# Kernel optimization log

Measured on AMD Instinct MI355X. Metric: run time of the kernel, lower is better.

## Reference

```python
import jax, jax.numpy as jnp
import numpy as np

B, N, F_IN, F_OUT, H = 8, 1024, 256, 256, 4
HD = F_OUT // H  # head_dim = 64
NEG_SLOPE = 0.2


def setup_inputs() -> dict:
    key = jax.random.key(0)
    k1, k2, k3 = jax.random.split(key, 3)
    x = jax.random.normal(k1, (B, N, F_IN), dtype=jnp.float32)
    adj = jnp.ones((B, N, N), dtype=jnp.int32)
    # Linear weight, stored as [in, out] so h = x @ W
    W = jax.random.normal(k2, (F_IN, F_OUT), dtype=jnp.float32) / np.sqrt(F_IN)
    # attention vector a: [H, 2*head_dim], xavier-ish init
    a = jax.random.normal(k3, (H, 2 * HD), dtype=jnp.float32) * np.sqrt(2.0 / (H + 2 * HD))
    return {"x": x, "adj": adj, "W": W, "a": a}


def reference(x, adj, W, a):
    Bq, Nq, _ = x.shape
    h = (x @ W).reshape(Bq, Nq, H, HD).transpose(0, 2, 1, 3)  # [B,H,N,HD]
    a1, a2 = a[:, :HD], a[:, HD:]  # decompose concat: e_nm = h_n.a1 + h_m.a2
    s1 = jnp.einsum('bhnd,hd->bhn', h, a1)
    s2 = jnp.einsum('bhmd,hd->bhm', h, a2)
    e = jax.nn.leaky_relu(s1[:, :, :, None] + s2[:, :, None, :], NEG_SLOPE)  # [B,H,N,N]
    e = jnp.where(adj[:, None, :, :] == 0, -jnp.inf, e)
    attention = jax.nn.softmax(e, axis=-1)
    out = jnp.einsum('bhnm,bhmd->bhnd', attention, h)
    return out.transpose(0, 2, 1, 3).reshape(Bq, Nq, H * HD)
```

## Files before the change

### kernel.cpp

```cpp
#include <hip/hip_runtime.h>
#include <math.h>

#define H 4
#define HD 64
#define NN 1024
#define BB 8
#define FIN 256
#define FOUT 256

typedef _Float16 f16x8 __attribute__((ext_vector_type(8)));
typedef _Float16 f16x4 __attribute__((ext_vector_type(4)));
typedef _Float16 f16x2 __attribute__((ext_vector_type(2)));
typedef float f32x4 __attribute__((ext_vector_type(4)));

__global__ __launch_bounds__(256) void prep(const int* __restrict__ adj,
                                            unsigned* __restrict__ adjP,
                                            const float* __restrict__ W,
                                            _Float16* __restrict__ WT) {
  __shared__ float tile[64][68];
  const int tid = threadIdx.x;
  if (blockIdx.x < 1024) {
    size_t widx = (size_t)blockIdx.x * 256 + tid;
    const int4* p = (const int4*)adj + widx * 8;
    int4 v[8];
#pragma unroll
    for (int i = 0; i < 8; ++i) v[i] = p[i];
    unsigned bits = 0;
#pragma unroll
    for (int i = 0; i < 8; ++i) {
      bits |= (v[i].x != 0 ? 1u : 0u) << (4 * i);
      bits |= (v[i].y != 0 ? 2u : 0u) << (4 * i);
      bits |= (v[i].z != 0 ? 4u : 0u) << (4 * i);
      bits |= (v[i].w != 0 ? 8u : 0u) << (4 * i);
    }
    adjP[widx] = bits;
  } else {
    const int bx = blockIdx.x - 1024;
    const int k0 = (bx & 3) * 64, f0 = (bx >> 2) * 64;
    const int r = tid >> 4, c4 = (tid & 15) * 4;
#pragma unroll
    for (int p = 0; p < 4; ++p) {
      float4 v = *(const float4*)&W[(size_t)(k0 + p * 16 + r) * FOUT + f0 + c4];
      *(float4*)&tile[p * 16 + r][c4] = v;
    }
    __syncthreads();
    const int f = tid >> 2, kg = (tid & 3) * 16;
#pragma unroll
    for (int i = 0; i < 4; ++i) {
      f16x4 o;
#pragma unroll
      for (int j = 0; j < 4; ++j) o[j] = (_Float16)tile[kg + i * 4 + j][f];
      *(f16x4*)&WT[(size_t)(f0 + f) * FIN + k0 + kg + i * 4] = o;
    }
  }
}

__global__ __launch_bounds__(256) void gemm_xw(const float* __restrict__ x,
                                               const _Float16* __restrict__ WT,
                                               const float* __restrict__ a,
                                               _Float16* __restrict__ hT,
                                               float* __restrict__ s1_ws,
                                               float* __restrict__ s2_ws,
                                               float* __restrict__ u_ws,
                                               float* __restrict__ v_ws) {
  __shared__ _Float16 xs[64][264];
  const int tid = threadIdx.x;
  const int lane = tid & 63, w = tid >> 6;
  const int c = lane & 15, q = lane >> 4;
  const int bn0 = blockIdx.x * 64;
  const int head = blockIdx.y;
  const int b = bn0 >> 10, nb = bn0 & 1023;
  const int bh = b * H + head;

  float4 v[16];
#pragma unroll
  for (int p = 0; p < 16; ++p) {
    int f = p * 256 + tid;
    int row = f >> 6, col = (f & 63) * 4;
    v[p] = *(const float4*)&x[(size_t)(bn0 + row) * FIN + col];
  }
#pragma unroll
  for (int p = 0; p < 16; ++p) {
    int f = p * 256 + tid;
    int row = f >> 6, col = (f & 63) * 4;
    f16x4 h4;
    h4[0] = (_Float16)v[p].x; h4[1] = (_Float16)v[p].y;
    h4[2] = (_Float16)v[p].z; h4[3] = (_Float16)v[p].w;
    *(f16x4*)&xs[row][col] = h4;
  }
  __syncthreads();

  f32x4 acc[4];
#pragma unroll
  for (int t = 0; t < 4; ++t) acc[t] = (f32x4){0.f, 0.f, 0.f, 0.f};
  const _Float16* wbase = WT + (size_t)head * 64 * FIN;
#pragma unroll
  for (int ks = 0; ks < 8; ++ks) {
    f16x8 af = *(const f16x8*)&xs[w * 16 + c][ks * 32 + q * 8];
#pragma unroll
    for (int t = 0; t < 4; ++t) {
      f16x8 bf = *(const f16x8*)&wbase[(size_t)(t * 16 + c) * FIN + ks * 32 + q * 8];
      acc[t] = __builtin_amdgcn_mfma_f32_16x16x32_f16(af, bf, acc[t], 0, 0, 0);
    }
  }

  float a1v[4], a2v[4];
#pragma unroll
  for (int t = 0; t < 4; ++t) {
    a1v[t] = a[head * 2 * HD + t * 16 + c];
    a2v[t] = a[head * 2 * HD + HD + t * 16 + c];
  }
  float s1p[4] = {0.f, 0.f, 0.f, 0.f};
  float s2p[4] = {0.f, 0.f, 0.f, 0.f};
#pragma unroll
  for (int t = 0; t < 4; ++t) {
    f16x4 hv;
#pragma unroll
    for (int rr = 0; rr < 4; ++rr) {
      hv[rr] = (_Float16)acc[t][rr];
      s1p[rr] += acc[t][rr] * a1v[t];
      s2p[rr] += acc[t][rr] * a2v[t];
    }
    *(f16x4*)&hT[((size_t)(bh * 64 + t * 16 + c)) * NN + nb + w * 16 + q * 4] = hv;
  }
#pragma unroll
  for (int rr = 0; rr < 4; ++rr) {
    float s1 = s1p[rr], s2 = s2p[rr];
#pragma unroll
    for (int off = 8; off; off >>= 1) {
      s1 += __shfl_xor(s1, off);
      s2 += __shfl_xor(s2, off);
    }
    if (c == 0) {
      int n = nb + w * 16 + q * 4 + rr;
      size_t idx = (size_t)bh * NN + n;
      s1_ws[idx] = s1;
      s2_ws[idx] = s2;
      u_ws[idx] = __expf(s2);
      v_ws[idx] = __expf(0.2f * s2);
    }
  }
}

__global__ __launch_bounds__(256) void attn(const _Float16* __restrict__ hT,
                                            const float* __restrict__ s1_ws,
                                            const float* __restrict__ s2_ws,
                                            const float* __restrict__ u_ws,
                                            const float* __restrict__ v_ws,
                                            const unsigned* __restrict__ adjP,
                                            float* __restrict__ out) {
  __shared__ float s2r[NN], uu[NN], vv[NN];
  __shared__ _Float16 pt[2][32][136];
  __shared__ unsigned adjW[32][32];
  __shared__ float invL[32];
  const int tid = threadIdx.x, lane = tid & 63, w = tid >> 6;
  const int c = lane & 15, q = lane >> 4;
  const int ntile = blockIdx.x, bh = blockIdx.y;
  const int b = bh >> 2, head = bh & 3;
  const int n0 = ntile * 32;

  {
    size_t base = (size_t)bh * NN + tid * 4;
    *(float4*)&s2r[tid * 4] = *(const float4*)&s2_ws[base];
    *(float4*)&uu[tid * 4] = *(const float4*)&u_ws[base];
    *(float4*)&vv[tid * 4] = *(const float4*)&v_ws[base];
    uint4 aw = *(const uint4*)&adjP[((size_t)(b * NN + n0)) * 32 + tid * 4];
    *(uint4*)&adjW[tid >> 3][(tid * 4) & 31] = aw;
  }
  __syncthreads();

  float s1v[8];
#pragma unroll
  for (int r = 0; r < 8; ++r) s1v[r] = s1_ws[(size_t)bh * NN + n0 + w * 8 + r];

  const int wc = lane >> 4;
  const int shft = (2 * lane) & 31;

  float mx[8];
#pragma unroll
  for (int r = 0; r < 8; ++r) mx[r] = -INFINITY;
#pragma unroll
  for (int ch = 0; ch < 8; ++ch) {
    float2 s2p = *(const float2*)&s2r[ch * 128 + 2 * lane];
#pragma unroll
    for (int r = 0; r < 8; ++r) {
      unsigned bits = adjW[w * 8 + r][ch * 4 + wc] >> shft;
      mx[r] = fmaxf(mx[r], (bits & 1u) ? s2p.x : -INFINITY);
      mx[r] = fmaxf(mx[r], (bits & 2u) ? s2p.y : -INFINITY);
    }
  }
  float Arow[8], Brow[8], ns1[8];
#pragma unroll
  for (int r = 0; r < 8; ++r) {
    float m = mx[r];
#pragma unroll
    for (int off = 32; off; off >>= 1) m = fmaxf(m, __shfl_xor(m, off));
    float t0 = s1v[r] + m;
    float M = fmaxf(t0, 0.2f * t0);
    Arow[r] = __expf(s1v[r] - M);
    Brow[r] = __expf(0.2f * s1v[r] - M);
    ns1[r] = -s1v[r];
  }

  float Lp[8];
#pragma unroll
  for (int r = 0; r < 8; ++r) Lp[r] = 0.f;
  f32x4 acc[2];
  acc[0] = (f32x4){0.f, 0.f, 0.f, 0.f};
  acc[1] = (f32x4){0.f, 0.f, 0.f, 0.f};
  const _Float16* bptr = hT + ((size_t)bh * 64 + w * 16 + c) * NN + q * 8;

  f16x8 nbf0 = *(const f16x8*)(bptr);
  f16x8 nbf1 = *(const f16x8*)(bptr + 32);
  f16x8 nbf2 = *(const f16x8*)(bptr + 64);
  f16x8 nbf3 = *(const f16x8*)(bptr + 96);

  for (int ch = 0; ch < 8; ++ch) {
    const int buf = ch & 1;
    f16x8 bf0 = nbf0, bf1 = nbf1, bf2 = nbf2, bf3 = nbf3;
    float2 s2p = *(const float2*)&s2r[ch * 128 + 2 * lane];
    float2 up = *(const float2*)&uu[ch * 128 + 2 * lane];
    float2 vp = *(const float2*)&vv[ch * 128 + 2 * lane];
#pragma unroll
    for (int r = 0; r < 8; ++r) {
      unsigned bits = adjW[w * 8 + r][ch * 4 + wc] >> shft;
      float p0 = (s2p.x >= ns1[r]) ? Arow[r] * up.x : Brow[r] * vp.x;
      float p1 = (s2p.y >= ns1[r]) ? Arow[r] * up.y : Brow[r] * vp.y;
      p0 = (bits & 1u) ? p0 : 0.f;
      p1 = (bits & 2u) ? p1 : 0.f;
      Lp[r] += p0 + p1;
      f16x2 pk = __builtin_bit_cast(f16x2, __builtin_amdgcn_cvt_pkrtz(p0, p1));
      *(f16x2*)&pt[buf][w * 8 + r][2 * lane] = pk;
    }
    if (ch < 7) {
      nbf0 = *(const f16x8*)(bptr + (ch + 1) * 128);
      nbf1 = *(const f16x8*)(bptr + (ch + 1) * 128 + 32);
      nbf2 = *(const f16x8*)(bptr + (ch + 1) * 128 + 64);
      nbf3 = *(const f16x8*)(bptr + (ch + 1) * 128 + 96);
    }
    __syncthreads();
#pragma unroll
    for (int t = 0; t < 2; ++t) {
      f16x8 a0 = *(const f16x8*)&pt[buf][t * 16 + c][q * 8];
      f16x8 a1 = *(const f16x8*)&pt[buf][t * 16 + c][32 + q * 8];
      f16x8 a2 = *(const f16x8*)&pt[buf][t * 16 + c][64 + q * 8];
      f16x8 a3 = *(const f16x8*)&pt[buf][t * 16 + c][96 + q * 8];
      acc[t] = __builtin_amdgcn_mfma_f32_16x16x32_f16(a0, bf0, acc[t], 0, 0, 0);
      acc[t] = __builtin_amdgcn_mfma_f32_16x16x32_f16(a1, bf1, acc[t], 0, 0, 0);
      acc[t] = __builtin_amdgcn_mfma_f32_16x16x32_f16(a2, bf2, acc[t], 0, 0, 0);
      acc[t] = __builtin_amdgcn_mfma_f32_16x16x32_f16(a3, bf3, acc[t], 0, 0, 0);
    }
  }

  float myL = 0.f;
#pragma unroll
  for (int r = 0; r < 8; ++r) {
    float s = Lp[r];
#pragma unroll
    for (int off = 32; off; off >>= 1) s += __shfl_xor(s, off);
    if (lane == r) myL = s;
  }
  if (lane < 8) invL[w * 8 + lane] = 1.0f / myL;
  __syncthreads();
#pragma unroll
  for (int t = 0; t < 2; ++t) {
#pragma unroll
    for (int rr = 0; rr < 4; ++rr) {
      int nloc = t * 16 + q * 4 + rr;
      out[((size_t)(b * NN + n0 + nloc)) * FOUT + head * 64 + w * 16 + c] =
          acc[t][rr] * invL[nloc];
    }
  }
}

extern "C" void kernel_launch(void* const* d_in, const int* in_sizes, int n_in,
                              void* d_out, int out_size, void* d_ws, size_t ws_size,
                              hipStream_t stream) {
  const float* x = (const float*)d_in[0];
  const int* adj = (const int*)d_in[1];
  const float* W = (const float*)d_in[2];
  const float* a = (const float*)d_in[3];
  float* out = (float*)d_out;

  char* ws = (char*)d_ws;
  _Float16* hT = (_Float16*)ws;
  _Float16* WT = (_Float16*)(ws + (size_t)4 * 1024 * 1024);
  float* s1_ws = (float*)(ws + (size_t)4 * 1024 * 1024 + 128 * 1024);
  float* s2_ws = s1_ws + (size_t)BB * H * NN;
  float* u_ws = s2_ws + (size_t)BB * H * NN;
  float* v_ws = u_ws + (size_t)BB * H * NN;
  unsigned* adjP = (unsigned*)(v_ws + (size_t)BB * H * NN);

  prep<<<1040, 256, 0, stream>>>(adj, adjP, W, WT);
  gemm_xw<<<dim3(128, 4), 256, 0, stream>>>(x, WT, a, hT, s1_ws, s2_ws, u_ws, v_ws);
  attn<<<dim3(32, 32), 256, 0, stream>>>(hT, s1_ws, s2_ws, u_ws, v_ws, adjP, out);
}
```

Baseline: 118.8 us.

## Fuse adjacency bit-packing into attention kernel and load x directly into registers

```diff
diff --git a/kernel.cpp b/kernel.cpp
--- a/kernel.cpp
+++ b/kernel.cpp
@@ -13,45 +13,26 @@
 typedef _Float16 f16x2 __attribute__((ext_vector_type(2)));
 typedef float f32x4 __attribute__((ext_vector_type(4)));
 
-__global__ __launch_bounds__(256) void prep(const int* __restrict__ adj,
-                                            unsigned* __restrict__ adjP,
-                                            const float* __restrict__ W,
-                                            _Float16* __restrict__ WT) {
+__global__ __launch_bounds__(256) void prep_w(const float* __restrict__ W,
+                                              _Float16* __restrict__ WT) {
   __shared__ float tile[64][68];
   const int tid = threadIdx.x;
-  if (blockIdx.x < 1024) {
-    size_t widx = (size_t)blockIdx.x * 256 + tid;
-    const int4* p = (const int4*)adj + widx * 8;
-    int4 v[8];
-#pragma unroll
-    for (int i = 0; i < 8; ++i) v[i] = p[i];
-    unsigned bits = 0;
-#pragma unroll
-    for (int i = 0; i < 8; ++i) {
-      bits |= (v[i].x != 0 ? 1u : 0u) << (4 * i);
-      bits |= (v[i].y != 0 ? 2u : 0u) << (4 * i);
-      bits |= (v[i].z != 0 ? 4u : 0u) << (4 * i);
-      bits |= (v[i].w != 0 ? 8u : 0u) << (4 * i);
-    }
-    adjP[widx] = bits;
-  } else {
-    const int bx = blockIdx.x - 1024;
-    const int k0 = (bx & 3) * 64, f0 = (bx >> 2) * 64;
-    const int r = tid >> 4, c4 = (tid & 15) * 4;
-#pragma unroll
-    for (int p = 0; p < 4; ++p) {
-      float4 v = *(const float4*)&W[(size_t)(k0 + p * 16 + r) * FOUT + f0 + c4];
-      *(float4*)&tile[p * 16 + r][c4] = v;
-    }
-    __syncthreads();
-    const int f = tid >> 2, kg = (tid & 3) * 16;
-#pragma unroll
-    for (int i = 0; i < 4; ++i) {
-      f16x4 o;
-#pragma unroll
-      for (int j = 0; j < 4; ++j) o[j] = (_Float16)tile[kg + i * 4 + j][f];
-      *(f16x4*)&WT[(size_t)(f0 + f) * FIN + k0 + kg + i * 4] = o;
-    }
+  const int bx = blockIdx.x;
+  const int k0 = (bx & 3) * 64, f0 = (bx >> 2) * 64;
+  const int r = tid >> 4, c4 = (tid & 15) * 4;
+#pragma unroll
+  for (int p = 0; p < 4; ++p) {
+    float4 v = *(const float4*)&W[(size_t)(k0 + p * 16 + r) * FOUT + f0 + c4];
+    *(float4*)&tile[p * 16 + r][c4] = v;
+  }
+  __syncthreads();
+  const int f = tid >> 2, kg = (tid & 3) * 16;
+#pragma unroll
+  for (int i = 0; i < 4; ++i) {
+    f16x4 o;
+#pragma unroll
+    for (int j = 0; j < 4; ++j) o[j] = (_Float16)tile[kg + i * 4 + j][f];
+    *(f16x4*)&WT[(size_t)(f0 + f) * FIN + k0 + kg + i * 4] = o;
   }
 }
 
@@ -63,7 +44,6 @@
                                                float* __restrict__ s2_ws,
                                                float* __restrict__ u_ws,
                                                float* __restrict__ v_ws) {
-  __shared__ _Float16 xs[64][264];
   const int tid = threadIdx.x;
   const int lane = tid & 63, w = tid >> 6;
   const int c = lane & 15, q = lane >> 4;
@@ -72,31 +52,28 @@
   const int b = bn0 >> 10, nb = bn0 & 1023;
   const int bh = b * H + head;
 
-  float4 v[16];
-#pragma unroll
-  for (int p = 0; p < 16; ++p) {
-    int f = p * 256 + tid;
-    int row = f >> 6, col = (f & 63) * 4;
-    v[p] = *(const float4*)&x[(size_t)(bn0 + row) * FIN + col];
-  }
-#pragma unroll
-  for (int p = 0; p < 16; ++p) {
-    int f = p * 256 + tid;
-    int row = f >> 6, col = (f & 63) * 4;
-    f16x4 h4;
-    h4[0] = (_Float16)v[p].x; h4[1] = (_Float16)v[p].y;
-    h4[2] = (_Float16)v[p].z; h4[3] = (_Float16)v[p].w;
-    *(f16x4*)&xs[row][col] = h4;
-  }
-  __syncthreads();
+  const _Float16* wbase = WT + (size_t)head * 64 * FIN;
+  const float* xrow = x + (size_t)(bn0 + w * 16 + c) * FIN;
+
+  float4 xa[16];
+#pragma unroll
+  for (int ks = 0; ks < 8; ++ks) {
+    xa[2 * ks] = *(const float4*)&xrow[ks * 32 + q * 8];
+    xa[2 * ks + 1] = *(const float4*)&xrow[ks * 32 + q * 8 + 4];
+  }
 
   f32x4 acc[4];
 #pragma unroll
   for (int t = 0; t < 4; ++t) acc[t] = (f32x4){0.f, 0.f, 0.f, 0.f};
-  const _Float16* wbase = WT + (size_t)head * 64 * FIN;
+
 #pragma unroll
   for (int ks = 0; ks < 8; ++ks) {
-    f16x8 af = *(const f16x8*)&xs[w * 16 + c][ks * 32 + q * 8];
+    float4 u0 = xa[2 * ks], u1 = xa[2 * ks + 1];
+    f16x8 af;
+    af[0] = (_Float16)u0.x; af[1] = (_Float16)u0.y;
+    af[2] = (_Float16)u0.z; af[3] = (_Float16)u0.w;
+    af[4] = (_Float16)u1.x; af[5] = (_Float16)u1.y;
+    af[6] = (_Float16)u1.z; af[7] = (_Float16)u1.w;
 #pragma unroll
     for (int t = 0; t < 4; ++t) {
       f16x8 bf = *(const f16x8*)&wbase[(size_t)(t * 16 + c) * FIN + ks * 32 + q * 8];
@@ -147,7 +124,7 @@
                                             const float* __restrict__ s2_ws,
                                             const float* __restrict__ u_ws,
                                             const float* __restrict__ v_ws,
-                                            const unsigned* __restrict__ adjP,
+                                            const int* __restrict__ adj,
                                             float* __restrict__ out) {
   __shared__ float s2r[NN], uu[NN], vv[NN];
   __shared__ _Float16 pt[2][32][136];
@@ -164,8 +141,27 @@
     *(float4*)&s2r[tid * 4] = *(const float4*)&s2_ws[base];
     *(float4*)&uu[tid * 4] = *(const float4*)&u_ws[base];
     *(float4*)&vv[tid * 4] = *(const float4*)&v_ws[base];
-    uint4 aw = *(const uint4*)&adjP[((size_t)(b * NN + n0)) * 32 + tid * 4];
-    *(uint4*)&adjW[tid >> 3][(tid * 4) & 31] = aw;
+  }
+  {
+    const int row = tid >> 3, seg = tid & 7;
+    const int4* ap = (const int4*)&adj[((size_t)(b * NN + n0 + row)) * NN + seg * 128];
+    unsigned wds[4];
+#pragma unroll
+    for (int wi = 0; wi < 4; ++wi) {
+      int4 vb[8];
+#pragma unroll
+      for (int i = 0; i < 8; ++i) vb[i] = ap[wi * 8 + i];
+      unsigned bits = 0;
+#pragma unroll
+      for (int i = 0; i < 8; ++i) {
+        bits |= (vb[i].x != 0 ? 1u : 0u) << (4 * i);
+        bits |= (vb[i].y != 0 ? 2u : 0u) << (4 * i);
+        bits |= (vb[i].z != 0 ? 4u : 0u) << (4 * i);
+        bits |= (vb[i].w != 0 ? 8u : 0u) << (4 * i);
+      }
+      wds[wi] = bits;
+    }
+    *(uint4*)&adjW[row][seg * 4] = make_uint4(wds[0], wds[1], wds[2], wds[3]);
   }
   __syncthreads();
 
@@ -289,9 +285,8 @@
   float* s2_ws = s1_ws + (size_t)BB * H * NN;
   float* u_ws = s2_ws + (size_t)BB * H * NN;
   float* v_ws = u_ws + (size_t)BB * H * NN;
-  unsigned* adjP = (unsigned*)(v_ws + (size_t)BB * H * NN);
-
-  prep<<<1040, 256, 0, stream>>>(adj, adjP, W, WT);
+
+  prep_w<<<16, 256, 0, stream>>>(W, WT);
   gemm_xw<<<dim3(128, 4), 256, 0, stream>>>(x, WT, a, hT, s1_ws, s2_ws, u_ws, v_ws);
-  attn<<<dim3(32, 32), 256, 0, stream>>>(hT, s1_ws, s2_ws, u_ws, v_ws, adjP, out);
-}
+  attn<<<dim3(32, 32), 256, 0, stream>>>(hT, s1_ws, s2_ws, u_ws, v_ws, adj, out);
+}
```

New measurement: 129.1 us. +8.6%, slower.

## Halve attention row tile to 16 and recompute exp(s2) in-kernel

Applied to the files above, without the earlier changes.

```diff
diff --git a/kernel.cpp b/kernel.cpp
--- a/kernel.cpp
+++ b/kernel.cpp
@@ -60,9 +60,7 @@
                                                const float* __restrict__ a,
                                                _Float16* __restrict__ hT,
                                                float* __restrict__ s1_ws,
-                                               float* __restrict__ s2_ws,
-                                               float* __restrict__ u_ws,
-                                               float* __restrict__ v_ws) {
+                                               float* __restrict__ s2_ws) {
   __shared__ _Float16 xs[64][264];
   const int tid = threadIdx.x;
   const int lane = tid & 63, w = tid >> 6;
@@ -136,8 +134,6 @@
       size_t idx = (size_t)bh * NN + n;
       s1_ws[idx] = s1;
       s2_ws[idx] = s2;
-      u_ws[idx] = __expf(s2);
-      v_ws[idx] = __expf(0.2f * s2);
     }
   }
 }
@@ -145,53 +141,48 @@
 __global__ __launch_bounds__(256) void attn(const _Float16* __restrict__ hT,
                                             const float* __restrict__ s1_ws,
                                             const float* __restrict__ s2_ws,
-                                            const float* __restrict__ u_ws,
-                                            const float* __restrict__ v_ws,
                                             const unsigned* __restrict__ adjP,
                                             float* __restrict__ out) {
-  __shared__ float s2r[NN], uu[NN], vv[NN];
-  __shared__ _Float16 pt[2][32][136];
-  __shared__ unsigned adjW[32][32];
-  __shared__ float invL[32];
+  __shared__ float s2r[NN];
+  __shared__ _Float16 pt[2][16][136];
+  __shared__ unsigned adjW[16][32];
+  __shared__ float invL[16];
   const int tid = threadIdx.x, lane = tid & 63, w = tid >> 6;
   const int c = lane & 15, q = lane >> 4;
   const int ntile = blockIdx.x, bh = blockIdx.y;
   const int b = bh >> 2, head = bh & 3;
-  const int n0 = ntile * 32;
-
-  {
-    size_t base = (size_t)bh * NN + tid * 4;
-    *(float4*)&s2r[tid * 4] = *(const float4*)&s2_ws[base];
-    *(float4*)&uu[tid * 4] = *(const float4*)&u_ws[base];
-    *(float4*)&vv[tid * 4] = *(const float4*)&v_ws[base];
+  const int n0 = ntile * 16;
+
+  *(float4*)&s2r[tid * 4] = *(const float4*)&s2_ws[(size_t)bh * NN + tid * 4];
+  if (tid < 128) {
     uint4 aw = *(const uint4*)&adjP[((size_t)(b * NN + n0)) * 32 + tid * 4];
     *(uint4*)&adjW[tid >> 3][(tid * 4) & 31] = aw;
   }
   __syncthreads();
 
-  float s1v[8];
-#pragma unroll
-  for (int r = 0; r < 8; ++r) s1v[r] = s1_ws[(size_t)bh * NN + n0 + w * 8 + r];
+  float s1v[4];
+#pragma unroll
+  for (int r = 0; r < 4; ++r) s1v[r] = s1_ws[(size_t)bh * NN + n0 + w * 4 + r];
 
   const int wc = lane >> 4;
   const int shft = (2 * lane) & 31;
 
-  float mx[8];
-#pragma unroll
-  for (int r = 0; r < 8; ++r) mx[r] = -INFINITY;
+  float mx[4];
+#pragma unroll
+  for (int r = 0; r < 4; ++r) mx[r] = -INFINITY;
 #pragma unroll
   for (int ch = 0; ch < 8; ++ch) {
     float2 s2p = *(const float2*)&s2r[ch * 128 + 2 * lane];
 #pragma unroll
-    for (int r = 0; r < 8; ++r) {
-      unsigned bits = adjW[w * 8 + r][ch * 4 + wc] >> shft;
+    for (int r = 0; r < 4; ++r) {
+      unsigned bits = adjW[w * 4 + r][ch * 4 + wc] >> shft;
       mx[r] = fmaxf(mx[r], (bits & 1u) ? s2p.x : -INFINITY);
       mx[r] = fmaxf(mx[r], (bits & 2u) ? s2p.y : -INFINITY);
     }
   }
-  float Arow[8], Brow[8], ns1[8];
-#pragma unroll
-  for (int r = 0; r < 8; ++r) {
+  float Arow[4], Brow[4], ns1[4];
+#pragma unroll
+  for (int r = 0; r < 4; ++r) {
     float m = mx[r];
 #pragma unroll
     for (int off = 32; off; off >>= 1) m = fmaxf(m, __shfl_xor(m, off));
@@ -202,12 +193,8 @@
     ns1[r] = -s1v[r];
   }
 
-  float Lp[8];
-#pragma unroll
-  for (int r = 0; r < 8; ++r) Lp[r] = 0.f;
-  f32x4 acc[2];
-  acc[0] = (f32x4){0.f, 0.f, 0.f, 0.f};
-  acc[1] = (f32x4){0.f, 0.f, 0.f, 0.f};
+  float Lp[4] = {0.f, 0.f, 0.f, 0.f};
+  f32x4 acc = (f32x4){0.f, 0.f, 0.f, 0.f};
   const _Float16* bptr = hT + ((size_t)bh * 64 + w * 16 + c) * NN + q * 8;
 
   f16x8 nbf0 = *(const f16x8*)(bptr);
@@ -219,18 +206,18 @@
     const int buf = ch & 1;
     f16x8 bf0 = nbf0, bf1 = nbf1, bf2 = nbf2, bf3 = nbf3;
     float2 s2p = *(const float2*)&s2r[ch * 128 + 2 * lane];
-    float2 up = *(const float2*)&uu[ch * 128 + 2 * lane];
-    float2 vp = *(const float2*)&vv[ch * 128 + 2 * lane];
-#pragma unroll
-    for (int r = 0; r < 8; ++r) {
-      unsigned bits = adjW[w * 8 + r][ch * 4 + wc] >> shft;
-      float p0 = (s2p.x >= ns1[r]) ? Arow[r] * up.x : Brow[r] * vp.x;
-      float p1 = (s2p.y >= ns1[r]) ? Arow[r] * up.y : Brow[r] * vp.y;
+    float ux = __expf(s2p.x), uy = __expf(s2p.y);
+    float vx = __expf(0.2f * s2p.x), vy = __expf(0.2f * s2p.y);
+#pragma unroll
+    for (int r = 0; r < 4; ++r) {
+      unsigned bits = adjW[w * 4 + r][ch * 4 + wc] >> shft;
+      float p0 = (s2p.x >= ns1[r]) ? Arow[r] * ux : Brow[r] * vx;
+      float p1 = (s2p.y >= ns1[r]) ? Arow[r] * uy : Brow[r] * vy;
       p0 = (bits & 1u) ? p0 : 0.f;
       p1 = (bits & 2u) ? p1 : 0.f;
       Lp[r] += p0 + p1;
       f16x2 pk = __builtin_bit_cast(f16x2, __builtin_amdgcn_cvt_pkrtz(p0, p1));
-      *(f16x2*)&pt[buf][w * 8 + r][2 * lane] = pk;
+      *(f16x2*)&pt[buf][w * 4 + r][2 * lane] = pk;
     }
     if (ch < 7) {
       nbf0 = *(const f16x8*)(bptr + (ch + 1) * 128);
@@ -239,37 +226,31 @@
       nbf3 = *(const f16x8*)(bptr + (ch + 1) * 128 + 96);
     }
     __syncthreads();
-#pragma unroll
-    for (int t = 0; t < 2; ++t) {
-      f16x8 a0 = *(const f16x8*)&pt[buf][t * 16 + c][q * 8];
-      f16x8 a1 = *(const f16x8*)&pt[buf][t * 16 + c][32 + q * 8];
-      f16x8 a2 = *(const f16x8*)&pt[buf][t * 16 + c][64 + q * 8];
-      f16x8 a3 = *(const f16x8*)&pt[buf][t * 16 + c][96 + q * 8];
-      acc[t] = __builtin_amdgcn_mfma_f32_16x16x32_f16(a0, bf0, acc[t], 0, 0, 0);
-      acc[t] = __builtin_amdgcn_mfma_f32_16x16x32_f16(a1, bf1, acc[t], 0, 0, 0);
-      acc[t] = __builtin_amdgcn_mfma_f32_16x16x32_f16(a2, bf2, acc[t], 0, 0, 0);
-      acc[t] = __builtin_amdgcn_mfma_f32_16x16x32_f16(a3, bf3, acc[t], 0, 0, 0);
-    }
+    f16x8 a0 = *(const f16x8*)&pt[buf][c][q * 8];
+    f16x8 a1 = *(const f16x8*)&pt[buf][c][32 + q * 8];
+    f16x8 a2 = *(const f16x8*)&pt[buf][c][64 + q * 8];
+    f16x8 a3 = *(const f16x8*)&pt[buf][c][96 + q * 8];
+    acc = __builtin_amdgcn_mfma_f32_16x16x32_f16(a0, bf0, acc, 0, 0, 0);
+    acc = __builtin_amdgcn_mfma_f32_16x16x32_f16(a1, bf1, acc, 0, 0, 0);
+    acc = __builtin_amdgcn_mfma_f32_16x16x32_f16(a2, bf2, acc, 0, 0, 0);
+    acc = __builtin_amdgcn_mfma_f32_16x16x32_f16(a3, bf3, acc, 0, 0, 0);
   }
 
   float myL = 0.f;
 #pragma unroll
-  for (int r = 0; r < 8; ++r) {
+  for (int r = 0; r < 4; ++r) {
     float s = Lp[r];
 #pragma unroll
     for (int off = 32; off; off >>= 1) s += __shfl_xor(s, off);
     if (lane == r) myL = s;
   }
-  if (lane < 8) invL[w * 8 + lane] = 1.0f / myL;
+  if (lane < 4) invL[w * 4 + lane] = 1.0f / myL;
   __syncthreads();
 #pragma unroll
-  for (int t = 0; t < 2; ++t) {
-#pragma unroll
-    for (int rr = 0; rr < 4; ++rr) {
-      int nloc = t * 16 + q * 4 + rr;
-      out[((size_t)(b * NN + n0 + nloc)) * FOUT + head * 64 + w * 16 + c] =
-          acc[t][rr] * invL[nloc];
-    }
+  for (int rr = 0; rr < 4; ++rr) {
+    int nloc = q * 4 + rr;
+    out[((size_t)(b * NN + n0 + nloc)) * FOUT + head * 64 + w * 16 + c] =
+        acc[rr] * invL[nloc];
   }
 }
 
@@ -287,11 +268,9 @@
   _Float16* WT = (_Float16*)(ws + (size_t)4 * 1024 * 1024);
   float* s1_ws = (float*)(ws + (size_t)4 * 1024 * 1024 + 128 * 1024);
   float* s2_ws = s1_ws + (size_t)BB * H * NN;
-  float* u_ws = s2_ws + (size_t)BB * H * NN;
-  float* v_ws = u_ws + (size_t)BB * H * NN;
-  unsigned* adjP = (unsigned*)(v_ws + (size_t)BB * H * NN);
+  unsigned* adjP = (unsigned*)(s2_ws + (size_t)BB * H * NN);
 
   prep<<<1040, 256, 0, stream>>>(adj, adjP, W, WT);
-  gemm_xw<<<dim3(128, 4), 256, 0, stream>>>(x, WT, a, hT, s1_ws, s2_ws, u_ws, v_ws);
-  attn<<<dim3(32, 32), 256, 0, stream>>>(hT, s1_ws, s2_ws, u_ws, v_ws, adjP, out);
-}
+  gemm_xw<<<dim3(128, 4), 256, 0, stream>>>(x, WT, a, hT, s1_ws, s2_ws);
+  attn<<<dim3(64, 32), 256, 0, stream>>>(hT, s1_ws, s2_ws, adjP, out);
+}
```

Result: slower. 129.2 us (+8.7%).

## Split attention over key dimension across waves with register-resident P operands

Applied to the files above, without the earlier changes.

```diff
diff --git a/kernel.cpp b/kernel.cpp
--- a/kernel.cpp
+++ b/kernel.cpp
@@ -150,125 +150,175 @@
                                             const unsigned* __restrict__ adjP,
                                             float* __restrict__ out) {
   __shared__ float s2r[NN], uu[NN], vv[NN];
-  __shared__ _Float16 pt[2][32][136];
-  __shared__ unsigned adjW[32][32];
-  __shared__ float invL[32];
+  __shared__ unsigned adjT[32][32];
+  __shared__ float accbuf[2][2][4][64][4];
+  __shared__ float Mbuf[4][32];
+  __shared__ float Lbuf[4][32];
+  __shared__ float invLb[32];
   const int tid = threadIdx.x, lane = tid & 63, w = tid >> 6;
   const int c = lane & 15, q = lane >> 4;
   const int ntile = blockIdx.x, bh = blockIdx.y;
   const int b = bh >> 2, head = bh & 3;
   const int n0 = ntile * 32;
+  const int K0 = w * 256, W0 = w * 8;
 
   {
     size_t base = (size_t)bh * NN + tid * 4;
     *(float4*)&s2r[tid * 4] = *(const float4*)&s2_ws[base];
     *(float4*)&uu[tid * 4] = *(const float4*)&u_ws[base];
     *(float4*)&vv[tid * 4] = *(const float4*)&v_ws[base];
-    uint4 aw = *(const uint4*)&adjP[((size_t)(b * NN + n0)) * 32 + tid * 4];
-    *(uint4*)&adjW[tid >> 3][(tid * 4) & 31] = aw;
-  }
-  __syncthreads();
-
-  float s1v[8];
-#pragma unroll
-  for (int r = 0; r < 8; ++r) s1v[r] = s1_ws[(size_t)bh * NN + n0 + w * 8 + r];
-
-  const int wc = lane >> 4;
-  const int shft = (2 * lane) & 31;
-
-  float mx[8];
-#pragma unroll
-  for (int r = 0; r < 8; ++r) mx[r] = -INFINITY;
-#pragma unroll
-  for (int ch = 0; ch < 8; ++ch) {
-    float2 s2p = *(const float2*)&s2r[ch * 128 + 2 * lane];
-#pragma unroll
-    for (int r = 0; r < 8; ++r) {
-      unsigned bits = adjW[w * 8 + r][ch * 4 + wc] >> shft;
-      mx[r] = fmaxf(mx[r], (bits & 1u) ? s2p.x : -INFINITY);
-      mx[r] = fmaxf(mx[r], (bits & 2u) ? s2p.y : -INFINITY);
-    }
-  }
-  float Arow[8], Brow[8], ns1[8];
-#pragma unroll
-  for (int r = 0; r < 8; ++r) {
-    float m = mx[r];
-#pragma unroll
-    for (int off = 32; off; off >>= 1) m = fmaxf(m, __shfl_xor(m, off));
-    float t0 = s1v[r] + m;
-    float M = fmaxf(t0, 0.2f * t0);
-    Arow[r] = __expf(s1v[r] - M);
-    Brow[r] = __expf(0.2f * s1v[r] - M);
-    ns1[r] = -s1v[r];
-  }
-
-  float Lp[8];
-#pragma unroll
-  for (int r = 0; r < 8; ++r) Lp[r] = 0.f;
-  f32x4 acc[2];
-  acc[0] = (f32x4){0.f, 0.f, 0.f, 0.f};
-  acc[1] = (f32x4){0.f, 0.f, 0.f, 0.f};
-  const _Float16* bptr = hT + ((size_t)bh * 64 + w * 16 + c) * NN + q * 8;
-
-  f16x8 nbf0 = *(const f16x8*)(bptr);
-  f16x8 nbf1 = *(const f16x8*)(bptr + 32);
-  f16x8 nbf2 = *(const f16x8*)(bptr + 64);
-  f16x8 nbf3 = *(const f16x8*)(bptr + 96);
-
-  for (int ch = 0; ch < 8; ++ch) {
-    const int buf = ch & 1;
-    f16x8 bf0 = nbf0, bf1 = nbf1, bf2 = nbf2, bf3 = nbf3;
-    float2 s2p = *(const float2*)&s2r[ch * 128 + 2 * lane];
-    float2 up = *(const float2*)&uu[ch * 128 + 2 * lane];
-    float2 vp = *(const float2*)&vv[ch * 128 + 2 * lane];
-#pragma unroll
-    for (int r = 0; r < 8; ++r) {
-      unsigned bits = adjW[w * 8 + r][ch * 4 + wc] >> shft;
-      float p0 = (s2p.x >= ns1[r]) ? Arow[r] * up.x : Brow[r] * vp.x;
-      float p1 = (s2p.y >= ns1[r]) ? Arow[r] * up.y : Brow[r] * vp.y;
-      p0 = (bits & 1u) ? p0 : 0.f;
-      p1 = (bits & 2u) ? p1 : 0.f;
-      Lp[r] += p0 + p1;
-      f16x2 pk = __builtin_bit_cast(f16x2, __builtin_amdgcn_cvt_pkrtz(p0, p1));
-      *(f16x2*)&pt[buf][w * 8 + r][2 * lane] = pk;
-    }
-    if (ch < 7) {
-      nbf0 = *(const f16x8*)(bptr + (ch + 1) * 128);
-      nbf1 = *(const f16x8*)(bptr + (ch + 1) * 128 + 32);
-      nbf2 = *(const f16x8*)(bptr + (ch + 1) * 128 + 64);
-      nbf3 = *(const f16x8*)(bptr + (ch + 1) * 128 + 96);
-    }
-    __syncthreads();
+    const int row = tid >> 3, wd0 = (tid & 7) * 4;
+    uint4 aw = *(const uint4*)&adjP[((size_t)(b * NN + n0 + row)) * 32 + wd0];
+    adjT[wd0 + 0][row] = aw.x;
+    adjT[wd0 + 1][row] = aw.y;
+    adjT[wd0 + 2][row] = aw.z;
+    adjT[wd0 + 3][row] = aw.w;
+  }
+  float s1A = s1_ws[(size_t)bh * NN + n0 + c];
+  float s1B = s1_ws[(size_t)bh * NN + n0 + 16 + c];
+  __syncthreads();
+
+  float mxA = -INFINITY, mxB = -INFINITY;
+#pragma unroll
+  for (int ks = 0; ks < 8; ++ks) {
+    int m0 = K0 + ks * 32 + q * 8;
+    f32x4 sa = *(const f32x4*)&s2r[m0];
+    f32x4 sb = *(const f32x4*)&s2r[m0 + 4];
+    unsigned wdA = adjT[W0 + ks][c] >> (q * 8);
+    unsigned wdB = adjT[W0 + ks][c + 16] >> (q * 8);
+#pragma unroll
+    for (int j = 0; j < 4; ++j) {
+      mxA = fmaxf(mxA, ((wdA >> j) & 1u) ? sa[j] : -INFINITY);
+      mxA = fmaxf(mxA, ((wdA >> (j + 4)) & 1u) ? sb[j] : -INFINITY);
+      mxB = fmaxf(mxB, ((wdB >> j) & 1u) ? sa[j] : -INFINITY);
+      mxB = fmaxf(mxB, ((wdB >> (j + 4)) & 1u) ? sb[j] : -INFINITY);
+    }
+  }
+  mxA = fmaxf(mxA, __shfl_xor(mxA, 16));
+  mxA = fmaxf(mxA, __shfl_xor(mxA, 32));
+  mxB = fmaxf(mxB, __shfl_xor(mxB, 16));
+  mxB = fmaxf(mxB, __shfl_xor(mxB, 32));
+  if (lane < 16) {
+    Mbuf[w][c] = mxA;
+    Mbuf[w][16 + c] = mxB;
+  }
+  __syncthreads();
+  float mrowA = fmaxf(fmaxf(Mbuf[0][c], Mbuf[1][c]), fmaxf(Mbuf[2][c], Mbuf[3][c]));
+  float mrowB = fmaxf(fmaxf(Mbuf[0][16 + c], Mbuf[1][16 + c]),
+                      fmaxf(Mbuf[2][16 + c], Mbuf[3][16 + c]));
+  float tA = s1A + mrowA, tB = s1B + mrowB;
+  float MA = fmaxf(tA, 0.2f * tA);
+  float MB = fmaxf(tB, 0.2f * tB);
+  float ArowA = __expf(s1A - MA), BrowA = __expf(0.2f * s1A - MA), ns1A = -s1A;
+  float ArowB = __expf(s1B - MB), BrowB = __expf(0.2f * s1B - MB), ns1B = -s1B;
+
+  float LpA = 0.f, LpB = 0.f;
+  f32x4 acc[2][4];
+#pragma unroll
+  for (int t = 0; t < 2; ++t)
+#pragma unroll
+    for (int d = 0; d < 4; ++d) acc[t][d] = (f32x4){0.f, 0.f, 0.f, 0.f};
+  const _Float16* hbase = hT + (size_t)bh * 64 * NN + (size_t)c * NN + K0 + q * 8;
+
+#pragma unroll 2
+  for (int ks = 0; ks < 8; ++ks) {
+    f16x8 bf0 = *(const f16x8*)(hbase + (size_t)0 * 16 * NN + ks * 32);
+    f16x8 bf1 = *(const f16x8*)(hbase + (size_t)1 * 16 * NN + ks * 32);
+    f16x8 bf2 = *(const f16x8*)(hbase + (size_t)2 * 16 * NN + ks * 32);
+    f16x8 bf3 = *(const f16x8*)(hbase + (size_t)3 * 16 * NN + ks * 32);
+
+    int m0 = K0 + ks * 32 + q * 8;
+    f32x4 sa = *(const f32x4*)&s2r[m0];
+    f32x4 sb = *(const f32x4*)&s2r[m0 + 4];
+    f32x4 ua = *(const f32x4*)&uu[m0];
+    f32x4 ub = *(const f32x4*)&uu[m0 + 4];
+    f32x4 va = *(const f32x4*)&vv[m0];
+    f32x4 vb = *(const f32x4*)&vv[m0 + 4];
+    unsigned wdA = adjT[W0 + ks][c] >> (q * 8);
+    unsigned wdB = adjT[W0 + ks][c + 16] >> (q * 8);
+
+    float pA[8], pB[8];
+#pragma unroll
+    for (int j = 0; j < 4; ++j) {
+      float a0 = (sa[j] >= ns1A) ? ArowA * ua[j] : BrowA * va[j];
+      float a1 = (sb[j] >= ns1A) ? ArowA * ub[j] : BrowA * vb[j];
+      pA[j] = ((wdA >> j) & 1u) ? a0 : 0.f;
+      pA[j + 4] = ((wdA >> (j + 4)) & 1u) ? a1 : 0.f;
+      float b0 = (sa[j] >= ns1B) ? ArowB * ua[j] : BrowB * va[j];
+      float b1 = (sb[j] >= ns1B) ? ArowB * ub[j] : BrowB * vb[j];
+      pB[j] = ((wdB >> j) & 1u) ? b0 : 0.f;
+      pB[j + 4] = ((wdB >> (j + 4)) & 1u) ? b1 : 0.f;
+    }
+    LpA += ((pA[0] + pA[1]) + (pA[2] + pA[3])) + ((pA[4] + pA[5]) + (pA[6] + pA[7]));
+    LpB += ((pB[0] + pB[1]) + (pB[2] + pB[3])) + ((pB[4] + pB[5]) + (pB[6] + pB[7]));
+
+    union { f16x8 v8; f16x2 h2[4]; } PA, PB;
+#pragma unroll
+    for (int j = 0; j < 4; ++j) {
+      PA.h2[j] = __builtin_bit_cast(f16x2, __builtin_amdgcn_cvt_pkrtz(pA[2 * j], pA[2 * j + 1]));
+      PB.h2[j] = __builtin_bit_cast(f16x2, __builtin_amdgcn_cvt_pkrtz(pB[2 * j], pB[2 * j + 1]));
+    }
+
+    acc[0][0] = __builtin_amdgcn_mfma_f32_16x16x32_f16(PA.v8, bf0, acc[0][0], 0, 0, 0);
+    acc[0][1] = __builtin_amdgcn_mfma_f32_16x16x32_f16(PA.v8, bf1, acc[0][1], 0, 0, 0);
+    acc[0][2] = __builtin_amdgcn_mfma_f32_16x16x32_f16(PA.v8, bf2, acc[0][2], 0, 0, 0);
+    acc[0][3] = __builtin_amdgcn_mfma_f32_16x16x32_f16(PA.v8, bf3, acc[0][3], 0, 0, 0);
+    acc[1][0] = __builtin_amdgcn_mfma_f32_16x16x32_f16(PB.v8, bf0, acc[1][0], 0, 0, 0);
+    acc[1][1] = __builtin_amdgcn_mfma_f32_16x16x32_f16(PB.v8, bf1, acc[1][1], 0, 0, 0);
+    acc[1][2] = __builtin_amdgcn_mfma_f32_16x16x32_f16(PB.v8, bf2, acc[1][2], 0, 0, 0);
+    acc[1][3] = __builtin_amdgcn_mfma_f32_16x16x32_f16(PB.v8, bf3, acc[1][3], 0, 0, 0);
+  }
+
+  LpA += __shfl_xor(LpA, 16);
+  LpA += __shfl_xor(LpA, 32);
+  LpB += __shfl_xor(LpB, 16);
+  LpB += __shfl_xor(LpB, 32);
+  if (lane < 16) {
+    Lbuf[w][c] = LpA;
+    Lbuf[w][16 + c] = LpB;
+  }
+  if (w >= 2) {
+#pragma unroll
+    for (int t = 0; t < 2; ++t)
+#pragma unroll
+      for (int d = 0; d < 4; ++d)
+        *(f32x4*)&accbuf[w - 2][t][d][lane][0] = acc[t][d];
+  }
+  __syncthreads();
+  if (w < 2) {
+#pragma unroll
+    for (int t = 0; t < 2; ++t)
+#pragma unroll
+      for (int d = 0; d < 4; ++d)
+        acc[t][d] += *(const f32x4*)&accbuf[w][t][d][lane][0];
+  }
+  if (tid < 32) {
+    float Ls = Lbuf[0][tid] + Lbuf[1][tid] + Lbuf[2][tid] + Lbuf[3][tid];
+    invLb[tid] = 1.0f / Ls;
+  }
+  __syncthreads();
+  if (w == 1) {
+#pragma unroll
+    for (int t = 0; t < 2; ++t)
+#pragma unroll
+      for (int d = 0; d < 4; ++d)
+        *(f32x4*)&accbuf[0][t][d][lane][0] = acc[t][d];
+  }
+  __syncthreads();
+  if (w == 0) {
 #pragma unroll
     for (int t = 0; t < 2; ++t) {
-      f16x8 a0 = *(const f16x8*)&pt[buf][t * 16 + c][q * 8];
-      f16x8 a1 = *(const f16x8*)&pt[buf][t * 16 + c][32 + q * 8];
-      f16x8 a2 = *(const f16x8*)&pt[buf][t * 16 + c][64 + q * 8];
-      f16x8 a3 = *(const f16x8*)&pt[buf][t * 16 + c][96 + q * 8];
-      acc[t] = __builtin_amdgcn_mfma_f32_16x16x32_f16(a0, bf0, acc[t], 0, 0, 0);
-      acc[t] = __builtin_amdgcn_mfma_f32_16x16x32_f16(a1, bf1, acc[t], 0, 0, 0);
-      acc[t] = __builtin_amdgcn_mfma_f32_16x16x32_f16(a2, bf2, acc[t], 0, 0, 0);
-      acc[t] = __builtin_amdgcn_mfma_f32_16x16x32_f16(a3, bf3, acc[t], 0, 0, 0);
-    }
-  }
-
-  float myL = 0.f;
-#pragma unroll
-  for (int r = 0; r < 8; ++r) {
-    float s = Lp[r];
-#pragma unroll
-    for (int off = 32; off; off >>= 1) s += __shfl_xor(s, off);
-    if (lane == r) myL = s;
-  }
-  if (lane < 8) invL[w * 8 + lane] = 1.0f / myL;
-  __syncthreads();
-#pragma unroll
-  for (int t = 0; t < 2; ++t) {
-#pragma unroll
-    for (int rr = 0; rr < 4; ++rr) {
-      int nloc = t * 16 + q * 4 + rr;
-      out[((size_t)(b * NN + n0 + nloc)) * FOUT + head * 64 + w * 16 + c] =
-          acc[t][rr] * invL[nloc];
+#pragma unroll
+      for (int d = 0; d < 4; ++d)
+        acc[t][d] += *(const f32x4*)&accbuf[0][t][d][lane][0];
+#pragma unroll
+      for (int rr = 0; rr < 4; ++rr) {
+        int nloc = t * 16 + q * 4 + rr;
+        float il = invLb[nloc];
+        size_t o = ((size_t)(b * NN + n0 + nloc)) * FOUT + head * 64;
+#pragma unroll
+        for (int d = 0; d < 4; ++d) out[o + d * 16 + c] = acc[t][d][rr] * il;
+      }
     }
   }
 }
```

After: 116.8 us. No clear change (-1.7%).
